# Kernel tuning notes

Measured on AMD Instinct MI355X. Metric: run time of the kernel, lower is better.

Reference implementation:

```python
import jax, jax.numpy as jnp
import numpy as np

NEG_SLOPE = 0.01  # torch LeakyReLU default

def leaky_relu(x):
    return jnp.where(x >= 0, x, NEG_SLOPE * x)

def setup_inputs() -> dict:
    key = jax.random.key(0)
    ks = jax.random.split(key, 12)
    D = 128
    N_U, N_I, E = 100000, 50000, 1000000
    s = 1.0 / np.sqrt(D)
    return {
        "h_user": jax.random.normal(ks[0], (N_U, D), jnp.float32),
        "h_item": jax.random.normal(ks[1], (N_I, D), jnp.float32),
        "src_idx": jax.random.randint(ks[2], (E,), 0, N_U, jnp.int64) if jax.config.jax_enable_x64 else jax.random.randint(ks[2], (E,), 0, N_U, jnp.int32),
        "dst_idx": jax.random.randint(ks[3], (E,), 0, N_I, jnp.int32),
        "W_left": jax.random.normal(ks[4], (D, D), jnp.float32) * s,
        "b_left": jax.random.normal(ks[5], (D,), jnp.float32) * s,
        "W_right": jax.random.normal(ks[6], (D, D), jnp.float32) * s,
        "b_right": jax.random.normal(ks[7], (D,), jnp.float32) * s,
        "W1": jax.random.normal(ks[8], (D, D), jnp.float32) * s,
        "b1": jax.random.normal(ks[9], (D,), jnp.float32) * s,
        "W2": jax.random.normal(ks[10], (D, 1), jnp.float32) * s,
        "b2": jax.random.normal(ks[11], (1,), jnp.float32) * s,
    }

def reference(h_user, h_item, src_idx, dst_idx,
              W_left, b_left, W_right, b_right, W1, b1, W2, b2):
    # node linear transforms (dropout is identity in eval mode)
    u_f = h_user @ W_left + b_left      # [N_u, D]
    i_f = h_item @ W_right + b_right    # [N_i, D]
    # edge gather + add (dgl fn.u_add_v)
    score = u_f[src_idx] + i_f[dst_idx]  # [E, D]
    # pred MLP: LeakyReLU -> Linear(D,D) -> LeakyReLU -> Linear(D,1) -> LeakyReLU
    x = leaky_relu(score)
    x = leaky_relu(x @ W1 + b1)
    x = leaky_relu(x @ W2 + b2)         # [E, 1]
    return x
```

## Files before the change

### kernel.cpp

```cpp
#include <hip/hip_runtime.h>

typedef __attribute__((ext_vector_type(8))) short bf16x8;
typedef __attribute__((ext_vector_type(4))) float f32x4;
typedef __attribute__((ext_vector_type(2))) float f32x2;

__device__ __forceinline__ float leaky(float v) { return fmaxf(v, 0.01f * v); }

__device__ __forceinline__ unsigned short f2bf(float a) {
    unsigned int u = __float_as_uint(a);
    return (unsigned short)((u + 0x7FFFu + ((u >> 16) & 1u)) >> 16);
}

__device__ __forceinline__ unsigned int cvtpk(float a, float b) {
#if __has_builtin(__builtin_amdgcn_cvt_pk_bf16_f32)
    typedef __attribute__((ext_vector_type(2))) __bf16 bf2_t;
    bf2_t v = __builtin_amdgcn_cvt_pk_bf16_f32(a, b);
    return __builtin_bit_cast(unsigned int, v);
#else
    unsigned int ua = __float_as_uint(a);
    ua = (ua + 0x7FFFu + ((ua >> 16) & 1u)) >> 16;
    unsigned int ub = __float_as_uint(b);
    ub = (ub + 0x7FFFu + ((ub >> 16) & 1u)) >> 16;
    return ua | (ub << 16);
#endif
}

__device__ __forceinline__ f32x2 unpk2(unsigned int d) {
    f32x2 r;
    r.x = __uint_as_float(d << 16);
    r.y = __uint_as_float(d & 0xFFFF0000u);
    return r;
}

__device__ __forceinline__ unsigned int mix1(unsigned int u, unsigned int i) {
    f32x2 v = unpk2(u) + unpk2(i);
    v = __builtin_elementwise_max(v, v * 0.01f);
    return cvtpk(v.x, v.y);
}

__global__ __launch_bounds__(128) void prep(const float* __restrict__ WL,
                                            const float* __restrict__ WR,
                                            const float* __restrict__ W1,
                                            unsigned short* __restrict__ WLf,
                                            unsigned short* __restrict__ WRf,
                                            unsigned short* __restrict__ Wf) {
    int g = blockIdx.x;
    int f = (g & 127) * 128 + threadIdx.x;
    int j = f & 7, lane = (f >> 3) & 63, nt = (f >> 9) & 7, kb = f >> 12;
    int n = nt * 16 + (lane & 15);
    int kf = kb * 32 + (lane >> 4) * 8 + j;
    if (g < 128) {
        WLf[f] = f2bf(WL[kf * 128 + n]);
    } else if (g < 256) {
        WRf[f] = f2bf(WR[kf * 128 + n]);
    } else {
        int k = (kf & 7) * 16 + (kf >> 3);
        Wf[f] = f2bf(W1[k * 128 + n]);
    }
}

#define PITCH 136

__global__ __launch_bounds__(256, 4) void node_mfma2(const float* __restrict__ h_user,
                                                     const float* __restrict__ h_item,
                                                     const unsigned short* __restrict__ WLf,
                                                     const unsigned short* __restrict__ WRf,
                                                     const float* __restrict__ b_left,
                                                     const float* __restrict__ b_right,
                                                     unsigned short* __restrict__ u_f,
                                                     unsigned short* __restrict__ i_f,
                                                     int N_U, int N_I, int BU) {
    bool isU = (int)blockIdx.x < BU;
    const float* h = isU ? h_user : h_item;
    const unsigned short* Wfr = isU ? WLf : WRf;
    const float* b = isU ? b_left : b_right;
    unsigned short* out = isU ? u_f : i_f;
    int N = isU ? N_U : N_I;
    int r0 = (isU ? blockIdx.x : blockIdx.x - BU) * 128;

    __shared__ unsigned short xt[128 * PITCH];
    int t = threadIdx.x;
    int s = t & 15;
    int el0 = t >> 4;
#pragma unroll
    for (int pass = 0; pass < 8; ++pass) {
        int el = pass * 16 + el0;
        int row = min(r0 + el, N - 1);
        const f32x4* hp = (const f32x4*)(h + (size_t)row * 128);
        f32x4 a0 = hp[s];
        f32x4 a1 = hp[s + 16];
        unsigned int* rp = (unsigned int*)(xt + el * PITCH);
        rp[2 * s]          = cvtpk(a0.x, a0.y);
        rp[2 * s + 1]      = cvtpk(a0.z, a0.w);
        rp[32 + 2 * s]     = cvtpk(a1.x, a1.y);
        rp[32 + 2 * s + 1] = cvtpk(a1.z, a1.w);
    }
    __syncthreads();

    int wave = t >> 6;
    int lane = t & 63;
    int m0 = wave * 32;
    int col = lane & 15;
    int quad = lane >> 4;

    f32x4 acc[2][8];
#pragma unroll
    for (int mt = 0; mt < 2; ++mt)
#pragma unroll
        for (int nt = 0; nt < 8; ++nt) acc[mt][nt] = (f32x4){0.f, 0.f, 0.f, 0.f};

#pragma unroll
    for (int kb = 0; kb < 4; ++kb) {
        bf16x8 afr[2];
#pragma unroll
        for (int mt = 0; mt < 2; ++mt)
            afr[mt] = *(const bf16x8*)(xt + (m0 + mt * 16 + col) * PITCH + kb * 32 + quad * 8);
#pragma unroll
        for (int nt = 0; nt < 8; ++nt) {
            bf16x8 bfr = *(const bf16x8*)(Wfr + ((kb * 8 + nt) * 64 + lane) * 8);
            acc[0][nt] = __builtin_amdgcn_mfma_f32_16x16x32_bf16(afr[0], bfr, acc[0][nt], 0, 0, 0);
            acc[1][nt] = __builtin_amdgcn_mfma_f32_16x16x32_bf16(afr[1], bfr, acc[1][nt], 0, 0, 0);
        }
    }

    float bb[8];
#pragma unroll
    for (int nt = 0; nt < 8; ++nt) bb[nt] = b[nt * 16 + col];
#pragma unroll
    for (int mt = 0; mt < 2; ++mt)
#pragma unroll
        for (int rr = 0; rr < 4; ++rr) {
            int row = r0 + m0 + mt * 16 + quad * 4 + rr;
            uint4 v;
            v.x = cvtpk(acc[mt][0][rr] + bb[0], acc[mt][1][rr] + bb[1]);
            v.y = cvtpk(acc[mt][2][rr] + bb[2], acc[mt][3][rr] + bb[3]);
            v.z = cvtpk(acc[mt][4][rr] + bb[4], acc[mt][5][rr] + bb[5]);
            v.w = cvtpk(acc[mt][6][rr] + bb[6], acc[mt][7][rr] + bb[7]);
            if (row < N) *(uint4*)(out + (size_t)row * 128 + col * 8) = v;
        }
}

#define TE 128

__global__ __launch_bounds__(512, 8) void edge_kernel(
    const unsigned short* __restrict__ u_f, const unsigned short* __restrict__ i_f,
    const int* __restrict__ src, const int* __restrict__ dst,
    const unsigned short* __restrict__ Wf,
    const float* __restrict__ b1, const float* __restrict__ W2,
    const float* __restrict__ b2, float* __restrict__ out, int E) {
    __shared__ unsigned short xt[TE * PITCH];
    __shared__ float zb[4][2][32];
    int t = threadIdx.x;
    int e0 = blockIdx.x * TE;

    int s = t & 15;
    int el0 = t >> 4;

    uint4 ug[4], ig[4];
#pragma unroll
    for (int pass = 0; pass < 4; ++pass) {
        int ec = min(e0 + pass * 32 + el0, E - 1);
        ug[pass] = *(const uint4*)(u_f + (size_t)src[ec] * 128 + s * 8);
        ig[pass] = *(const uint4*)(i_f + (size_t)dst[ec] * 128 + s * 8);
    }
#pragma unroll
    for (int pass = 0; pass < 4; ++pass) {
        int el = pass * 32 + el0;
        uint4 a;
        a.x = mix1(ug[pass].x, ig[pass].x);
        a.y = mix1(ug[pass].y, ig[pass].y);
        a.z = mix1(ug[pass].z, ig[pass].z);
        a.w = mix1(ug[pass].w, ig[pass].w);
        *(uint4*)(xt + el * PITCH + s * 8) = a;
    }
    __syncthreads();

    int wave = t >> 6;
    int lane = t & 63;
    int col = lane & 15;
    int quad = lane >> 4;
    int wp = wave >> 1;
    int ch = wave & 1;
    int m0 = wp * 32;

    f32x4 acc[2][4];
#pragma unroll
    for (int mt = 0; mt < 2; ++mt)
#pragma unroll
        for (int i = 0; i < 4; ++i) acc[mt][i] = (f32x4){0.f, 0.f, 0.f, 0.f};

#pragma unroll
    for (int kb = 0; kb < 4; ++kb) {
        bf16x8 afr[2];
#pragma unroll
        for (int mt = 0; mt < 2; ++mt)
            afr[mt] = *(const bf16x8*)(xt + (m0 + mt * 16 + col) * PITCH + kb * 32 + quad * 8);
#pragma unroll
        for (int i = 0; i < 4; ++i) {
            int nt = ch * 4 + i;
            bf16x8 bfr = *(const bf16x8*)(Wf + ((kb * 8 + nt) * 64 + lane) * 8);
            acc[0][i] = __builtin_amdgcn_mfma_f32_16x16x32_bf16(afr[0], bfr, acc[0][i], 0, 0, 0);
            acc[1][i] = __builtin_amdgcn_mfma_f32_16x16x32_bf16(afr[1], bfr, acc[1][i], 0, 0, 0);
        }
    }

    f32x4 p[2];
#pragma unroll
    for (int mt = 0; mt < 2; ++mt) p[mt] = (f32x4){0.f, 0.f, 0.f, 0.f};

#pragma unroll
    for (int i = 0; i < 4; ++i) {
        int n = (ch * 4 + i) * 16 + col;
        float bb = b1[n];
        float ww = W2[n];
#pragma unroll
        for (int mt = 0; mt < 2; ++mt) {
            f32x4 y = acc[mt][i] + bb;
            y = __builtin_elementwise_max(y, y * 0.01f);
            p[mt] += y * ww;
        }
    }
#pragma unroll
    for (int off = 1; off < 16; off <<= 1)
#pragma unroll
        for (int mt = 0; mt < 2; ++mt)
#pragma unroll
            for (int rr = 0; rr < 4; ++rr) p[mt][rr] += __shfl_xor(p[mt][rr], off, 64);

    if (col == 0) {
#pragma unroll
        for (int mt = 0; mt < 2; ++mt)
#pragma unroll
            for (int rr = 0; rr < 4; ++rr)
                zb[wp][ch][mt * 16 + quad * 4 + rr] = p[mt][rr];
    }
    __syncthreads();

    if (t < 128) {
        int g = t >> 5;
        int idx = t & 31;
        float z = zb[g][0][idx] + zb[g][1][idx] + b2[0];
        int e = e0 + g * 32 + idx;
        if (e < E) out[e] = leaky(z);
    }
}

extern "C" void kernel_launch(void* const* d_in, const int* in_sizes, int n_in,
                              void* d_out, int out_size, void* d_ws, size_t ws_size,
                              hipStream_t stream) {
    const float* h_user  = (const float*)d_in[0];
    const float* h_item  = (const float*)d_in[1];
    const int*   src_idx = (const int*)d_in[2];
    const int*   dst_idx = (const int*)d_in[3];
    const float* W_left  = (const float*)d_in[4];
    const float* b_left  = (const float*)d_in[5];
    const float* W_right = (const float*)d_in[6];
    const float* b_right = (const float*)d_in[7];
    const float* W1      = (const float*)d_in[8];
    const float* b1      = (const float*)d_in[9];
    const float* W2      = (const float*)d_in[10];
    const float* b2      = (const float*)d_in[11];
    float* out = (float*)d_out;

    int N_U = in_sizes[0] / 128;
    int N_I = in_sizes[1] / 128;
    int E   = in_sizes[2];

    unsigned short* Wf  = (unsigned short*)d_ws;
    unsigned short* WLf = Wf + 16384;
    unsigned short* WRf = WLf + 16384;
    unsigned short* u_f = (unsigned short*)((char*)d_ws + 131072);
    unsigned short* i_f = u_f + (size_t)N_U * 128;

    prep<<<384, 128, 0, stream>>>(W_left, W_right, W1, WLf, WRf, Wf);

    int BU = (N_U + 127) / 128;
    int BI = (N_I + 127) / 128;
    node_mfma2<<<BU + BI, 256, 0, stream>>>(h_user, h_item, WLf, WRf, b_left, b_right,
                                            u_f, i_f, N_U, N_I, BU);

    edge_kernel<<<(E + TE - 1) / TE, 512, 0, stream>>>(u_f, i_f, src_idx, dst_idx,
                                                       Wf, b1, W2, b2, out, E);
}
```

Measured before the change: 232.4 us.

## Make edge kernel persistent with W1 fragments held in registers

The edge kernel becomes a grid-stride persistent kernel with at most 512 blocks, each looping over 128-edge tiles. Each block loads its W1 MFMA B-fragments into registers once, instead of reloading them from global memory for every tile. The launch-bounds occupancy hint drops from 8 to 4 to leave room for the extra registers. The aim is to cut block launch overhead and repeated weight loads. The cost is fewer resident waves to hide the latency of the random gathers, since no prefetch of the next tile is added.

```diff
diff --git a/kernel.cpp b/kernel.cpp
--- a/kernel.cpp
+++ b/kernel.cpp
@@ -142,38 +142,17 @@
 
 #define TE 128
 
-__global__ __launch_bounds__(512, 8) void edge_kernel(
+__global__ __launch_bounds__(512, 4) void edge_kernel(
     const unsigned short* __restrict__ u_f, const unsigned short* __restrict__ i_f,
     const int* __restrict__ src, const int* __restrict__ dst,
     const unsigned short* __restrict__ Wf,
     const float* __restrict__ b1, const float* __restrict__ W2,
-    const float* __restrict__ b2, float* __restrict__ out, int E) {
+    const float* __restrict__ b2, float* __restrict__ out, int E, int ntiles) {
     __shared__ unsigned short xt[TE * PITCH];
     __shared__ float zb[4][2][32];
     int t = threadIdx.x;
-    int e0 = blockIdx.x * TE;
-
     int s = t & 15;
     int el0 = t >> 4;
-
-    uint4 ug[4], ig[4];
-#pragma unroll
-    for (int pass = 0; pass < 4; ++pass) {
-        int ec = min(e0 + pass * 32 + el0, E - 1);
-        ug[pass] = *(const uint4*)(u_f + (size_t)src[ec] * 128 + s * 8);
-        ig[pass] = *(const uint4*)(i_f + (size_t)dst[ec] * 128 + s * 8);
-    }
-#pragma unroll
-    for (int pass = 0; pass < 4; ++pass) {
-        int el = pass * 32 + el0;
-        uint4 a;
-        a.x = mix1(ug[pass].x, ig[pass].x);
-        a.y = mix1(ug[pass].y, ig[pass].y);
-        a.z = mix1(ug[pass].z, ig[pass].z);
-        a.w = mix1(ug[pass].w, ig[pass].w);
-        *(uint4*)(xt + el * PITCH + s * 8) = a;
-    }
-    __syncthreads();
 
     int wave = t >> 6;
     int lane = t & 63;
@@ -183,65 +162,95 @@
     int ch = wave & 1;
     int m0 = wp * 32;
 
-    f32x4 acc[2][4];
-#pragma unroll
-    for (int mt = 0; mt < 2; ++mt)
-#pragma unroll
-        for (int i = 0; i < 4; ++i) acc[mt][i] = (f32x4){0.f, 0.f, 0.f, 0.f};
-
-#pragma unroll
-    for (int kb = 0; kb < 4; ++kb) {
-        bf16x8 afr[2];
+    bf16x8 breg[4][4];
+#pragma unroll
+    for (int kb = 0; kb < 4; ++kb)
+#pragma unroll
+        for (int i = 0; i < 4; ++i)
+            breg[kb][i] = *(const bf16x8*)(Wf + ((kb * 8 + ch * 4 + i) * 64 + lane) * 8);
+
+    for (int tile = blockIdx.x; tile < ntiles; tile += gridDim.x) {
+        int e0 = tile * TE;
+
+        int ec[4];
+#pragma unroll
+        for (int pass = 0; pass < 4; ++pass)
+            ec[pass] = min(e0 + pass * 32 + el0, E - 1);
+        uint4 ug[4], ig[4];
+#pragma unroll
+        for (int pass = 0; pass < 4; ++pass) {
+            ug[pass] = *(const uint4*)(u_f + (size_t)src[ec[pass]] * 128 + s * 8);
+            ig[pass] = *(const uint4*)(i_f + (size_t)dst[ec[pass]] * 128 + s * 8);
+        }
+#pragma unroll
+        for (int pass = 0; pass < 4; ++pass) {
+            uint4 a;
+            a.x = mix1(ug[pass].x, ig[pass].x);
+            a.y = mix1(ug[pass].y, ig[pass].y);
+            a.z = mix1(ug[pass].z, ig[pass].z);
+            a.w = mix1(ug[pass].w, ig[pass].w);
+            *(uint4*)(xt + (pass * 32 + el0) * PITCH + s * 8) = a;
+        }
+        __syncthreads();
+
+        f32x4 acc[2][4];
 #pragma unroll
         for (int mt = 0; mt < 2; ++mt)
-            afr[mt] = *(const bf16x8*)(xt + (m0 + mt * 16 + col) * PITCH + kb * 32 + quad * 8);
+#pragma unroll
+            for (int i = 0; i < 4; ++i) acc[mt][i] = (f32x4){0.f, 0.f, 0.f, 0.f};
+
+#pragma unroll
+        for (int kb = 0; kb < 4; ++kb) {
+            bf16x8 afr[2];
+#pragma unroll
+            for (int mt = 0; mt < 2; ++mt)
+                afr[mt] = *(const bf16x8*)(xt + (m0 + mt * 16 + col) * PITCH + kb * 32 + quad * 8);
+#pragma unroll
+            for (int i = 0; i < 4; ++i) {
+                acc[0][i] = __builtin_amdgcn_mfma_f32_16x16x32_bf16(afr[0], breg[kb][i], acc[0][i], 0, 0, 0);
+                acc[1][i] = __builtin_amdgcn_mfma_f32_16x16x32_bf16(afr[1], breg[kb][i], acc[1][i], 0, 0, 0);
+            }
+        }
+
+        f32x4 p[2];
+#pragma unroll
+        for (int mt = 0; mt < 2; ++mt) p[mt] = (f32x4){0.f, 0.f, 0.f, 0.f};
+
 #pragma unroll
         for (int i = 0; i < 4; ++i) {
-            int nt = ch * 4 + i;
-            bf16x8 bfr = *(const bf16x8*)(Wf + ((kb * 8 + nt) * 64 + lane) * 8);
-            acc[0][i] = __builtin_amdgcn_mfma_f32_16x16x32_bf16(afr[0], bfr, acc[0][i], 0, 0, 0);
-            acc[1][i] = __builtin_amdgcn_mfma_f32_16x16x32_bf16(afr[1], bfr, acc[1][i], 0, 0, 0);
-        }
-    }
-
-    f32x4 p[2];
-#pragma unroll
-    for (int mt = 0; mt < 2; ++mt) p[mt] = (f32x4){0.f, 0.f, 0.f, 0.f};
-
-#pragma unroll
-    for (int i = 0; i < 4; ++i) {
-        int n = (ch * 4 + i) * 16 + col;
-        float bb = b1[n];
-        float ww = W2[n];
-#pragma unroll
-        for (int mt = 0; mt < 2; ++mt) {
-            f32x4 y = acc[mt][i] + bb;
-            y = __builtin_elementwise_max(y, y * 0.01f);
-            p[mt] += y * ww;
-        }
-    }
-#pragma unroll
-    for (int off = 1; off < 16; off <<= 1)
-#pragma unroll
-        for (int mt = 0; mt < 2; ++mt)
-#pragma unroll
-            for (int rr = 0; rr < 4; ++rr) p[mt][rr] += __shfl_xor(p[mt][rr], off, 64);
-
-    if (col == 0) {
-#pragma unroll
-        for (int mt = 0; mt < 2; ++mt)
-#pragma unroll
-            for (int rr = 0; rr < 4; ++rr)
-                zb[wp][ch][mt * 16 + quad * 4 + rr] = p[mt][rr];
-    }
-    __syncthreads();
-
-    if (t < 128) {
-        int g = t >> 5;
-        int idx = t & 31;
-        float z = zb[g][0][idx] + zb[g][1][idx] + b2[0];
-        int e = e0 + g * 32 + idx;
-        if (e < E) out[e] = leaky(z);
+            int n = (ch * 4 + i) * 16 + col;
+            float bb = b1[n];
+            float ww = W2[n];
+#pragma unroll
+            for (int mt = 0; mt < 2; ++mt) {
+                f32x4 y = acc[mt][i] + bb;
+                y = __builtin_elementwise_max(y, y * 0.01f);
+                p[mt] += y * ww;
+            }
+        }
+#pragma unroll
+        for (int off = 1; off < 16; off <<= 1)
+#pragma unroll
+            for (int mt = 0; mt < 2; ++mt)
+#pragma unroll
+                for (int rr = 0; rr < 4; ++rr) p[mt][rr] += __shfl_xor(p[mt][rr], off, 64);
+
+        if (col == 0) {
+#pragma unroll
+            for (int mt = 0; mt < 2; ++mt)
+#pragma unroll
+                for (int rr = 0; rr < 4; ++rr)
+                    zb[wp][ch][mt * 16 + quad * 4 + rr] = p[mt][rr];
+        }
+        __syncthreads();
+
+        if (t < 128) {
+            int g = t >> 5;
+            int idx = t & 31;
+            float z = zb[g][0][idx] + zb[g][1][idx] + b2[0];
+            int e = e0 + g * 32 + idx;
+            if (e < E) out[e] = leaky(z);
+        }
     }
 }
 
@@ -279,6 +288,8 @@
     node_mfma2<<<BU + BI, 256, 0, stream>>>(h_user, h_item, WLf, WRf, b_left, b_right,
                                             u_f, i_f, N_U, N_I, BU);
 
-    edge_kernel<<<(E + TE - 1) / TE, 512, 0, stream>>>(u_f, i_f, src_idx, dst_idx,
-                                                       Wf, b1, W2, b2, out, E);
-}
+    int ntiles = (E + TE - 1) / TE;
+    int grid = ntiles < 512 ? ntiles : 512;
+    edge_kernel<<<grid, 512, 0, stream>>>(u_f, i_f, src_idx, dst_idx,
+                                          Wf, b1, W2, b2, out, E, ntiles);
+}
```

After: 311.4 us. 1.34x slower.
